# Kernel tuning notes

Measured on AMD Instinct MI355X. Metric: run time of the kernel, lower is better.

The kernel has to match this reference:

```python
import jax, jax.numpy as jnp
import numpy as np

NU, MI, D, H, DH, L, LAYERS = 80000, 40000, 64, 8, 8, 2, 3
EUI, EII, DT, DI, B = 1600000, 400000, 768, 512, 512


def setup_inputs() -> dict:
    rng = np.random.default_rng(0)
    u = rng.integers(0, NU, EUI); it = rng.integers(0, MI, EUI)
    du = np.maximum(np.bincount(u, minlength=NU), 1)
    di = np.maximum(np.bincount(it, minlength=MI), 1)
    val = (1.0 / np.sqrt(du[u] * di[it])).astype(np.float32)
    g_row = np.concatenate([u, it + NU]).astype(np.int32)
    g_col = np.concatenate([it + NU, u]).astype(np.int32)
    g_val = np.concatenate([val, val])

    def ig(seed):  # random item-item graph + self loops (dgl.add_self_loop)
        r = np.random.default_rng(seed)
        s = r.integers(0, MI, EII); d = r.integers(0, MI, EII); sl = np.arange(MI)
        return np.concatenate([s, sl]).astype(np.int32), np.concatenate([d, sl]).astype(np.int32)
    t_src, t_dst = ig(1); i_src, i_dst = ig(2)

    def xav(*shape):
        lim = np.sqrt(6.0 / (shape[-2] + shape[-1]))
        return rng.uniform(-lim, lim, shape).astype(np.float32)

    inp = dict(
        user_emb=(rng.standard_normal((NU, D)) * 0.1).astype(np.float32),
        item_emb=(rng.standard_normal((MI, D)) * 0.1).astype(np.float32),
        g_row=g_row, g_col=g_col, g_val=g_val,
        txt_feat=rng.standard_normal((MI, DT)).astype(np.float32),
        img_feat=rng.standard_normal((MI, DI)).astype(np.float32),
        t_src=t_src, t_dst=t_dst, i_src=i_src, i_dst=i_dst,
        txt_proj_w=xav(DT, D), txt_proj_b=np.zeros(D, np.float32),
        txt_fc_w=xav(L, D, D), txt_attn_l=xav(L, H, DH), txt_attn_r=xav(L, H, DH),
        txt_bias=np.zeros((L, D), np.float32),
        img_proj_w=xav(DI, D), img_proj_b=np.zeros(D, np.float32),
        img_fc_w=xav(L, D, D), img_attn_l=xav(L, H, DH), img_attn_r=xav(L, H, DH),
        img_bias=np.zeros((L, D), np.float32),
        delta_img=xav(D, D), delta_txt=xav(D, D),
        alpha=np.float32(0.05), beta=np.float32(0.8),
        ln_g=np.ones(D, np.float32), ln_b=np.zeros(D, np.float32),
        users=rng.integers(0, NU, B).astype(np.int32),
    )
    return {k: jnp.asarray(v) for k, v in inp.items()}


def _spmm(row, col, val, x, n):
    return jax.ops.segment_sum(val[:, None] * x[col], row, num_segments=n)


def _gat_layer(x, src, dst, fc_w, al, ar, b):
    N = x.shape[0]
    h = (x @ fc_w).reshape(N, H, DH)                 # [N,H,Dh]
    el = jnp.einsum('nhd,hd->nh', h, al)
    er = jnp.einsum('nhd,hd->nh', h, ar)
    e = jax.nn.leaky_relu(el[src] + er[dst], 0.2)    # [E,H]
    m = jax.ops.segment_max(e, dst, num_segments=N)
    a = jnp.exp(e - m[dst])
    a = a / jax.ops.segment_sum(a, dst, num_segments=N)[dst]
    out = jax.ops.segment_sum(a[:, :, None] * h[src], dst, num_segments=N)
    return (out + b.reshape(1, H, DH)).reshape(N, H * DH)


def _branch(feat, src, dst, pw, pb, fcw, al, ar, bias):
    x = feat @ pw + pb
    for l in range(L):
        x = jax.nn.leaky_relu(_gat_layer(x, src, dst, fcw[l], al[l], ar[l], bias[l]), 0.2)
    return x


def _sinkhorn(C, eps=0.01, iters=100):
    K = jnp.exp(-C / eps)
    d1, d2 = C.shape
    mu = jnp.full((d1,), 1.0 / d1, C.dtype)
    nu = jnp.full((d2,), 1.0 / d2, C.dtype)
    def body(_, uv):
        u, v = uv
        u = mu / (K @ v + 1e-8)
        v = nu / (K.T @ u + 1e-8)
        return (u, v)
    u, v = jax.lax.fori_loop(0, iters, body, (mu, nu))
    return u[:, None] * K * v[None, :]


def _ot_align(mm, st, delta):
    I = mm.shape[0]
    # mean_i (mm[i,k]-st[i,l])^2 * scale, without materializing [I,D,D]
    C = ((mm * mm).mean(0)[:, None] + (st * st).mean(0)[None, :] - 2.0 * (mm.T @ st) / I) * 100.0
    T = jax.lax.stop_gradient(_sinkhorn(C))  # torch computes T under no_grad
    return mm @ (T + delta)


def reference(user_emb, item_emb, g_row, g_col, g_val, txt_feat, img_feat,
              t_src, t_dst, i_src, i_dst,
              txt_proj_w, txt_proj_b, txt_fc_w, txt_attn_l, txt_attn_r, txt_bias,
              img_proj_w, img_proj_b, img_fc_w, img_attn_l, img_attn_r, img_bias,
              delta_img, delta_txt, alpha, beta, ln_g, ln_b, users):
    # LightGCN propagation
    cur = jnp.concatenate([user_emb, item_emb], 0)
    acc = cur
    for _ in range(LAYERS):
        cur = _spmm(g_row, g_col, g_val, cur, NU + MI)
        acc = acc + cur
    light = acc / (LAYERS + 1)
    zu, zi_cf = light[:NU], light[NU:]
    # multimodal GAT branches (dropout = eval mode)
    zi_txt = _branch(txt_feat, t_src, t_dst, txt_proj_w, txt_proj_b, txt_fc_w, txt_attn_l, txt_attn_r, txt_bias)
    zi_img = _branch(img_feat, i_src, i_dst, img_proj_w, img_proj_b, img_fc_w, img_attn_l, img_attn_r, img_bias)
    # OAT fusion
    a_img = _ot_align(zi_img, zi_cf, delta_img)
    a_txt = _ot_align(zi_txt, zi_cf, delta_txt)
    z = (1.0 - alpha - beta) * zi_cf + alpha * a_img + beta * a_txt
    mu = z.mean(-1, keepdims=True)
    var = ((z - mu) ** 2).mean(-1, keepdims=True)
    z = (z - mu) / jnp.sqrt(var + 1e-5) * ln_g + ln_b
    z = z / jnp.maximum(jnp.linalg.norm(z, axis=-1, keepdims=True), 1e-12)
    return zu[users] @ z.T  # [B, M_items] ratings
```

## Files before the change

kernel.cpp:

```cpp
#include <hip/hip_runtime.h>
#include <math.h>

__device__ __forceinline__ float lrelu(float x) { return x >= 0.f ? x : 0.2f * x; }

__global__ void hist2_k(const int* __restrict__ d0, const int* __restrict__ d1,
                        int* __restrict__ t0, int* __restrict__ t1, int E) {
  int e = blockIdx.x * 256 + threadIdx.x;
  if (e >= E) return;
  if (blockIdx.y == 0)
    atomicAdd(&t0[d0[e]], 1);
  else
    atomicAdd(&t1[d1[e]], 1);
}

__global__ __launch_bounds__(256) void scan_part2_k(const int* __restrict__ t0,
                                                    const int* __restrict__ t1,
                                                    int* __restrict__ p0,
                                                    int* __restrict__ p1, int N) {
  const int* tick = blockIdx.y ? t1 : t0;
  int* part = blockIdx.y ? p1 : p0;
  __shared__ int red[256];
  int base = blockIdx.x * 4096;
  int s = 0;
  for (int i = threadIdx.x; i < 4096; i += 256) {
    int idx = base + i;
    if (idx < N) s += tick[idx];
  }
  red[threadIdx.x] = s;
  __syncthreads();
  for (int off = 128; off > 0; off >>= 1) {
    if (threadIdx.x < off) red[threadIdx.x] += red[threadIdx.x + off];
    __syncthreads();
  }
  if (threadIdx.x == 0) part[blockIdx.x] = red[0];
}

__global__ __launch_bounds__(1024) void scan_partials2_k(int* __restrict__ p0,
                                                         int* __restrict__ p1, int nb) {
  int* part = blockIdx.y ? p1 : p0;
  __shared__ int sh[1024];
  int t = threadIdx.x;
  int v = (t < nb) ? part[t] : 0;
  sh[t] = v;
  __syncthreads();
  for (int off = 1; off < 1024; off <<= 1) {
    int x = sh[t];
    int y = (t >= off) ? sh[t - off] : 0;
    __syncthreads();
    sh[t] = x + y;
    __syncthreads();
  }
  if (t < nb) part[t] = (t == 0) ? 0 : sh[t - 1];
  if (t == 0) part[nb] = sh[nb - 1];
}

__global__ __launch_bounds__(256) void scan_apply2_k(int* __restrict__ t0, int* __restrict__ t1,
                                                     int* __restrict__ r0, int* __restrict__ r1,
                                                     const int* __restrict__ p0,
                                                     const int* __restrict__ p1, int N, int nb) {
  int* tick = blockIdx.y ? t1 : t0;
  int* rs = blockIdx.y ? r1 : r0;
  const int* part = blockIdx.y ? p1 : p0;
  __shared__ int th[256];
  int base = blockIdx.x * 4096;
  int lo = base + threadIdx.x * 16;
  int vals[16];
  int s = 0;
#pragma unroll
  for (int j = 0; j < 16; ++j) {
    int idx = lo + j;
    int v = (idx < N) ? tick[idx] : 0;
    vals[j] = v;
    s += v;
  }
  th[threadIdx.x] = s;
  __syncthreads();
  for (int off = 1; off < 256; off <<= 1) {
    int x = th[threadIdx.x];
    int y = (threadIdx.x >= off) ? th[threadIdx.x - off] : 0;
    __syncthreads();
    th[threadIdx.x] = x + y;
    __syncthreads();
  }
  int excl = (threadIdx.x == 0) ? 0 : th[threadIdx.x - 1];
  int run = part[blockIdx.x] + excl;
#pragma unroll
  for (int j = 0; j < 16; ++j) {
    int idx = lo + j;
    if (idx < N) {
      rs[idx] = run;
      tick[idx] = run;
      run += vals[j];
    }
  }
  if (blockIdx.x == 0 && threadIdx.x == 0) rs[N] = part[nb];
}

__global__ void scatter_src2_k(const int* __restrict__ s0, const int* __restrict__ d0,
                               const int* __restrict__ s1, const int* __restrict__ d1,
                               int* __restrict__ t0, int* __restrict__ t1,
                               int* __restrict__ o0, int* __restrict__ o1, int E) {
  int e = blockIdx.x * 256 + threadIdx.x;
  if (e >= E) return;
  if (blockIdx.y == 0) {
    int pos = atomicAdd(&t0[d0[e]], 1);
    o0[pos] = s0[e];
  } else {
    int pos = atomicAdd(&t1[d1[e]], 1);
    o1[pos] = s1[e];
  }
}

#define NBUCK_MAX 512

__global__ __launch_bounds__(256) void bin_count_k(const int* __restrict__ row,
                                                   int* __restrict__ bcnt, int E, int nbuck) {
  __shared__ int h[NBUCK_MAX];
  for (int i = threadIdx.x; i < nbuck; i += 256) h[i] = 0;
  __syncthreads();
  int base = blockIdx.x * 4096;
#pragma unroll
  for (int j = 0; j < 16; ++j) {
    int e = base + j * 256 + threadIdx.x;
    if (e < E) atomicAdd(&h[row[e] >> 8], 1);
  }
  __syncthreads();
  for (int i = threadIdx.x; i < nbuck; i += 256) {
    int c = h[i];
    if (c) atomicAdd(&bcnt[i], c);
  }
}

__global__ __launch_bounds__(512) void bucket_scan_k(int* __restrict__ base,
                                                     int* __restrict__ btick, int nbuck) {
  __shared__ int sh[512];
  int t = threadIdx.x;
  int v = (t < nbuck) ? base[t] : 0;
  sh[t] = v;
  __syncthreads();
  for (int off = 1; off < 512; off <<= 1) {
    int x = sh[t];
    int y = (t >= off) ? sh[t - off] : 0;
    __syncthreads();
    sh[t] = x + y;
    __syncthreads();
  }
  if (t < nbuck) {
    int excl = sh[t] - v;
    base[t] = excl;
    btick[t * 16] = excl;
    if (t == nbuck - 1) base[nbuck] = sh[t];
  }
}

__global__ __launch_bounds__(256) void bin_scatter_k(const int* __restrict__ row,
                                                     const int* __restrict__ col,
                                                     const float* __restrict__ val,
                                                     int* __restrict__ btick,
                                                     int* __restrict__ binned, int E, int nbuck) {
  __shared__ int cnt[NBUCK_MAX];
  __shared__ int bbase[NBUCK_MAX];
  for (int i = threadIdx.x; i < nbuck; i += 256) cnt[i] = 0;
  __syncthreads();
  int base = blockIdx.x * 4096;
  int erow[16], rk[16];
#pragma unroll
  for (int j = 0; j < 16; ++j) {
    int e = base + j * 256 + threadIdx.x;
    if (e < E) {
      int r = row[e];
      erow[j] = r;
      rk[j] = atomicAdd(&cnt[r >> 8], 1);
    } else {
      erow[j] = -1;
    }
  }
  __syncthreads();
  for (int i = threadIdx.x; i < nbuck; i += 256) {
    int c = cnt[i];
    bbase[i] = c ? atomicAdd(&btick[i * 16], c) : 0;
  }
  __syncthreads();
#pragma unroll
  for (int j = 0; j < 16; ++j) {
    int e = base + j * 256 + threadIdx.x;
    if (e < E) {
      int r = erow[j];
      int pos = bbase[r >> 8] + rk[j];
      int* p = binned + (size_t)pos * 3;
      p[0] = r;
      p[1] = col[e];
      p[2] = __float_as_int(val[e]);
    }
  }
}

__global__ __launch_bounds__(256) void csr_build_k(const int* __restrict__ bbase,
                                                   const int* __restrict__ binned,
                                                   int* __restrict__ rs,
                                                   int2* __restrict__ cv, int NT) {
  __shared__ int lh[256];
  __shared__ int tmp[256];
  int b = blockIdx.x;
  int t = threadIdx.x;
  int r0 = b << 8;
  int e0 = bbase[b], e1 = bbase[b + 1];
  lh[t] = 0;
  __syncthreads();
  for (int e = e0 + t; e < e1; e += 256) {
    int r = binned[(size_t)e * 3];
    atomicAdd(&lh[r - r0], 1);
  }
  __syncthreads();
  int c = lh[t];
  tmp[t] = c;
  __syncthreads();
  for (int off = 1; off < 256; off <<= 1) {
    int x = tmp[t];
    int y = (t >= off) ? tmp[t - off] : 0;
    __syncthreads();
    tmp[t] = x + y;
    __syncthreads();
  }
  int pos0 = e0 + tmp[t] - c;
  lh[t] = pos0;
  int r = r0 + t;
  if (r < NT) rs[r] = pos0;
  if (t == 0 && b == gridDim.x - 1) rs[NT] = e1;
  __syncthreads();
  for (int e = e0 + t; e < e1; e += 256) {
    const int* p = binned + (size_t)e * 3;
    int rr = p[0];
    int cc = p[1];
    int vv = p[2];
    int pos = atomicAdd(&lh[rr - r0], 1);
    cv[pos] = make_int2(cc, vv);
  }
}

template <int MODE>
__global__ __launch_bounds__(256) void spmm_csr(const int* __restrict__ rs,
                                                const int2* __restrict__ cv,
                                                const float* __restrict__ xs,
                                                const float* __restrict__ ue,
                                                const float* __restrict__ ie, int NUx,
                                                const float* __restrict__ l1,
                                                float* __restrict__ outp, int NT, int wid0) {
  int wid = wid0 + blockIdx.x * 4 + (threadIdx.x >> 6);
  int lane = threadIdx.x & 63;
  if (wid >= NT) return;
  int g = lane >> 4, sl = lane & 15;
  int e0 = rs[wid], e1 = rs[wid + 1];
  double ax = 0.0, ay = 0.0, az = 0.0, aw = 0.0;
  int e = e0;
#define GATHER_PTR(cx)                                                             \
  (MODE == 1 ? ((cx) < NUx ? (const float4*)ue + (size_t)(cx)*16                   \
                           : (const float4*)ie + (size_t)((cx)-NUx) * 16)          \
             : (const float4*)xs + (size_t)(cx)*16)
#define ACC4(vv, xx)                                                               \
  {                                                                                \
    double dv = (double)(vv);                                                      \
    ax += dv * (double)(xx).x;                                                     \
    ay += dv * (double)(xx).y;                                                     \
    az += dv * (double)(xx).z;                                                     \
    aw += dv * (double)(xx).w;                                                     \
  }
  for (; e + 16 <= e1; e += 16) {
    int2 c0 = cv[e + g];
    int2 c1 = cv[e + 4 + g];
    int2 c2 = cv[e + 8 + g];
    int2 c3 = cv[e + 12 + g];
    float4 x0 = GATHER_PTR(c0.x)[sl];
    float4 x1 = GATHER_PTR(c1.x)[sl];
    float4 x2 = GATHER_PTR(c2.x)[sl];
    float4 x3 = GATHER_PTR(c3.x)[sl];
    ACC4(__int_as_float(c0.y), x0);
    ACC4(__int_as_float(c1.y), x1);
    ACC4(__int_as_float(c2.y), x2);
    ACC4(__int_as_float(c3.y), x3);
  }
  for (; e + 4 <= e1; e += 4) {
    int2 c0 = cv[e + g];
    float4 x0 = GATHER_PTR(c0.x)[sl];
    ACC4(__int_as_float(c0.y), x0);
  }
  if (e < e1) {
    int idx = e + g;
    int2 c0 = make_int2(0, 0);
    if (idx < e1) c0 = cv[idx];
    float4 x0 = GATHER_PTR(c0.x)[sl];
    ACC4(__int_as_float(c0.y), x0);
  }
#undef ACC4
#undef GATHER_PTR
  ax += __shfl_xor(ax, 16, 64); ay += __shfl_xor(ay, 16, 64);
  az += __shfl_xor(az, 16, 64); aw += __shfl_xor(aw, 16, 64);
  ax += __shfl_xor(ax, 32, 64); ay += __shfl_xor(ay, 32, 64);
  az += __shfl_xor(az, 32, 64); aw += __shfl_xor(aw, 32, 64);
  if (g == 0) {
    size_t ro = (size_t)wid * 16 + sl;
    float4 s4 = make_float4((float)ax, (float)ay, (float)az, (float)aw);
    if (MODE == 2) {
      float4 x0 = (wid < NUx) ? ((const float4*)ue)[(size_t)wid * 16 + sl]
                              : ((const float4*)ie)[(size_t)(wid - NUx) * 16 + sl];
      float4 f1 = ((const float4*)l1)[ro];
      float4 f2 = ((const float4*)xs)[ro];
      float4 o;
      o.x = (x0.x + f1.x + f2.x + s4.x) * 0.25f;
      o.y = (x0.y + f1.y + f2.y + s4.y) * 0.25f;
      o.z = (x0.z + f1.z + f2.z + s4.z) * 0.25f;
      o.w = (x0.w + f1.w + f2.w + s4.w) * 0.25f;
      ((float4*)outp)[ro] = o;
    } else {
      ((float4*)outp)[ro] = s4;
    }
  }
}

__global__ __launch_bounds__(256) void user_light_k(const int* __restrict__ rs,
                                                    const int2* __restrict__ cv,
                                                    const float* __restrict__ l2,
                                                    const float* __restrict__ ue,
                                                    const float* __restrict__ l1,
                                                    const int* __restrict__ users,
                                                    float* __restrict__ zu, int B) {
  int w = blockIdx.x * 4 + (threadIdx.x >> 6);
  int lane = threadIdx.x & 63;
  if (w >= B) return;
  int u = users[w];
  int g = lane >> 4, sl = lane & 15;
  int e0 = rs[u], e1 = rs[u + 1];
  double ax = 0.0, ay = 0.0, az = 0.0, aw = 0.0;
  int e = e0;
  for (; e + 4 <= e1; e += 4) {
    int2 c0 = cv[e + g];
    float4 x0 = ((const float4*)l2 + (size_t)c0.x * 16)[sl];
    double dv = (double)__int_as_float(c0.y);
    ax += dv * (double)x0.x; ay += dv * (double)x0.y;
    az += dv * (double)x0.z; aw += dv * (double)x0.w;
  }
  if (e < e1) {
    int idx = e + g;
    int2 c0 = make_int2(0, 0);
    if (idx < e1) c0 = cv[idx];
    float4 x0 = ((const float4*)l2 + (size_t)c0.x * 16)[sl];
    double dv = (double)__int_as_float(c0.y);
    ax += dv * (double)x0.x; ay += dv * (double)x0.y;
    az += dv * (double)x0.z; aw += dv * (double)x0.w;
  }
  ax += __shfl_xor(ax, 16, 64); ay += __shfl_xor(ay, 16, 64);
  az += __shfl_xor(az, 16, 64); aw += __shfl_xor(aw, 16, 64);
  ax += __shfl_xor(ax, 32, 64); ay += __shfl_xor(ay, 32, 64);
  az += __shfl_xor(az, 32, 64); aw += __shfl_xor(aw, 32, 64);
  if (g == 0) {
    size_t ro = (size_t)u * 16 + sl;
    float4 x0 = ((const float4*)ue)[ro];
    float4 f1 = ((const float4*)l1)[ro];
    float4 f2 = ((const float4*)l2)[ro];
    float4 o;
    o.x = (x0.x + f1.x + f2.x + (float)ax) * 0.25f;
    o.y = (x0.y + f1.y + f2.y + (float)ay) * 0.25f;
    o.z = (x0.z + f1.z + f2.z + (float)az) * 0.25f;
    o.w = (x0.w + f1.w + f2.w + (float)aw) * 0.25f;
    ((float4*)zu)[(size_t)w * 16 + sl] = o;
  }
}

template <int ACT>
__global__ __launch_bounds__(256) void gemm2_n64(const float* __restrict__ A0,
                                                 const float* __restrict__ A1,
                                                 const float* __restrict__ W0,
                                                 const float* __restrict__ W1,
                                                 const float* __restrict__ b0,
                                                 const float* __restrict__ b1,
                                                 float* __restrict__ C0,
                                                 float* __restrict__ C1, int M, int K0, int K1) {
  const float* A = blockIdx.y ? A1 : A0;
  const float* W = blockIdx.y ? W1 : W0;
  const float* bias = blockIdx.y ? b1 : b0;
  float* C = blockIdx.y ? C1 : C0;
  const int K = blockIdx.y ? K1 : K0;
  __shared__ float AsT[32][132];
  __shared__ float Ws[32][64];
  int t = threadIdx.x;
  int row0 = blockIdx.x * 128;
  int tr = t >> 4, tc = t & 15;
  int lr = t >> 1, lq = (t & 1) * 16;
  int wk = t >> 3, wc = (t & 7) * 8;
  float acc[8][4] = {};
  for (int k0 = 0; k0 < K; k0 += 32) {
    float a16[16];
    if (row0 + lr < M) {
      const float* src = A + (size_t)(row0 + lr) * K + k0 + lq;
#pragma unroll
      for (int j = 0; j < 16; j += 4) {
        float4 v = *(const float4*)(src + j);
        a16[j] = v.x; a16[j + 1] = v.y; a16[j + 2] = v.z; a16[j + 3] = v.w;
      }
    } else {
#pragma unroll
      for (int i = 0; i < 16; ++i) a16[i] = 0.f;
    }
    float4 w0 = *(const float4*)(W + (size_t)(k0 + wk) * 64 + wc);
    float4 w1 = *(const float4*)(W + (size_t)(k0 + wk) * 64 + wc + 4);
    __syncthreads();
#pragma unroll
    for (int i = 0; i < 16; ++i) AsT[lq + i][lr] = a16[i];
    *(float4*)&Ws[wk][wc] = w0;
    *(float4*)&Ws[wk][wc + 4] = w1;
    __syncthreads();
#pragma unroll
    for (int kki = 0; kki < 32; ++kki) {
      float4 av0 = *(const float4*)&AsT[kki][tr * 8];
      float4 av1 = *(const float4*)&AsT[kki][tr * 8 + 4];
      float4 wv = *(const float4*)&Ws[kki][tc * 4];
      acc[0][0] += av0.x * wv.x; acc[0][1] += av0.x * wv.y;
      acc[0][2] += av0.x * wv.z; acc[0][3] += av0.x * wv.w;
      acc[1][0] += av0.y * wv.x; acc[1][1] += av0.y * wv.y;
      acc[1][2] += av0.y * wv.z; acc[1][3] += av0.y * wv.w;
      acc[2][0] += av0.z * wv.x; acc[2][1] += av0.z * wv.y;
      acc[2][2] += av0.z * wv.z; acc[2][3] += av0.z * wv.w;
      acc[3][0] += av0.w * wv.x; acc[3][1] += av0.w * wv.y;
      acc[3][2] += av0.w * wv.z; acc[3][3] += av0.w * wv.w;
      acc[4][0] += av1.x * wv.x; acc[4][1] += av1.x * wv.y;
      acc[4][2] += av1.x * wv.z; acc[4][3] += av1.x * wv.w;
      acc[5][0] += av1.y * wv.x; acc[5][1] += av1.y * wv.y;
      acc[5][2] += av1.y * wv.z; acc[5][3] += av1.y * wv.w;
      acc[6][0] += av1.z * wv.x; acc[6][1] += av1.z * wv.y;
      acc[6][2] += av1.z * wv.z; acc[6][3] += av1.z * wv.w;
      acc[7][0] += av1.w * wv.x; acc[7][1] += av1.w * wv.y;
      acc[7][2] += av1.w * wv.z; acc[7][3] += av1.w * wv.w;
    }
  }
  float bv[4] = {0.f, 0.f, 0.f, 0.f};
  if (bias) *(float4*)bv = *(const float4*)(bias + tc * 4);
#pragma unroll
  for (int j = 0; j < 8; ++j) {
    int row = row0 + tr * 8 + j;
    if (row < M) {
      float o[4];
#pragma unroll
      for (int c = 0; c < 4; ++c) {
        float x = acc[j][c] + bv[c];
        o[c] = ACT ? lrelu(x) : x;
      }
      *(float4*)(C + (size_t)row * 64 + tc * 4) = *(float4*)o;
    }
  }
}

__global__ void attn2_scores(const float* __restrict__ h0, const float* __restrict__ h1,
                             const float* __restrict__ al0, const float* __restrict__ al1,
                             const float* __restrict__ ar0, const float* __restrict__ ar1,
                             float* __restrict__ el0, float* __restrict__ el1,
                             float* __restrict__ er0, float* __restrict__ er1, int N) {
  long t = (long)blockIdx.x * blockDim.x + threadIdx.x;
  if (t >= (long)N * 8) return;
  const float* h = blockIdx.y ? h1 : h0;
  const float* al = blockIdx.y ? al1 : al0;
  const float* ar = blockIdx.y ? ar1 : ar0;
  float* el = blockIdx.y ? el1 : el0;
  float* er = blockIdx.y ? er1 : er0;
  int n = (int)(t >> 3), hh = (int)(t & 7);
  const float4* hp = (const float4*)(h + (size_t)n * 64 + hh * 8);
  float4 hv0 = hp[0], hv1 = hp[1];
  const float4* ap = (const float4*)(al + hh * 8);
  float4 a0 = ap[0], a1 = ap[1];
  const float4* bp = (const float4*)(ar + hh * 8);
  float4 b0 = bp[0], b1 = bp[1];
  float sl = hv0.x * a0.x + hv0.y * a0.y + hv0.z * a0.z + hv0.w * a0.w +
             hv1.x * a1.x + hv1.y * a1.y + hv1.z * a1.z + hv1.w * a1.w;
  float sr = hv0.x * b0.x + hv0.y * b0.y + hv0.z * b0.z + hv0.w * b0.w +
             hv1.x * b1.x + hv1.y * b1.y + hv1.z * b1.z + hv1.w * b1.w;
  el[t] = sl;
  er[t] = sr;
}

__global__ __launch_bounds__(256) void gat_agg2(const int* __restrict__ rsa,
                                                const int* __restrict__ rsb,
                                                const int* __restrict__ sa,
                                                const int* __restrict__ sb,
                                                const float* __restrict__ ela,
                                                const float* __restrict__ elb,
                                                const float* __restrict__ era,
                                                const float* __restrict__ erb,
                                                const float* __restrict__ ha,
                                                const float* __restrict__ hbp,
                                                const float* __restrict__ ba,
                                                const float* __restrict__ bb,
                                                float* __restrict__ oa,
                                                float* __restrict__ ob, int N) {
  int br = blockIdx.y;
  const int* rs = br ? rsb : rsa;
  const int* srcs = br ? sb : sa;
  const float* el = br ? elb : ela;
  const float* er = br ? erb : era;
  const float* h = br ? hbp : ha;
  const float* bias = br ? bb : ba;
  float* out = br ? ob : oa;
  int d = blockIdx.x * 4 + (threadIdx.x >> 6);
  int lane = threadIdx.x & 63;
  if (d >= N) return;
  int hh = lane >> 3;
  int e0 = rs[d], e1 = rs[d + 1];
  float erd = er[(size_t)d * 8 + hh];
  double den = 0.0, acc = 0.0;
  int e = e0;
  for (; e + 8 <= e1; e += 8) {
    int s8[8];
#pragma unroll
    for (int j = 0; j < 8; ++j) s8[j] = srcs[e + j];
    float v8[8];
#pragma unroll
    for (int j = 0; j < 8; ++j) v8[j] = el[(size_t)s8[j] * 8 + hh];
    float h8[8];
#pragma unroll
    for (int j = 0; j < 8; ++j) h8[j] = h[(size_t)s8[j] * 64 + lane];
#pragma unroll
    for (int j = 0; j < 8; ++j) {
      float a = expf(lrelu(v8[j] + erd));
      den += (double)a;
      acc += (double)a * (double)h8[j];
    }
  }
  for (; e < e1; ++e) {
    int s = srcs[e];
    float a = expf(lrelu(el[(size_t)s * 8 + hh] + erd));
    den += (double)a;
    acc += (double)a * (double)h[(size_t)s * 64 + lane];
  }
  out[(size_t)d * 64 + lane] = lrelu((float)(acc / den) + bias[lane]);
}

__global__ __launch_bounds__(256) void gram_part_k(const float* __restrict__ mm0,
                                                   const float* __restrict__ mm1,
                                                   const float* __restrict__ st,
                                                   float* __restrict__ part, int N) {
  __shared__ float ms[128][64];
  __shared__ float ss[128][64];
  const float* mm = blockIdx.y ? mm1 : mm0;
  float* po = part + ((size_t)blockIdx.y * gridDim.x + blockIdx.x) * 4224;
  int t = threadIdx.x;
  int n0 = blockIdx.x * 128;
  for (int idx = t; idx < 128 * 16; idx += 256) {
    int r = idx >> 4, q = (idx & 15) * 4;
    float4 a, b;
    if (n0 + r < N) {
      a = *(const float4*)(mm + (size_t)(n0 + r) * 64 + q);
      b = *(const float4*)(st + (size_t)(n0 + r) * 64 + q);
    } else {
      a = make_float4(0, 0, 0, 0);
      b = make_float4(0, 0, 0, 0);
    }
    *(float4*)&ms[r][q] = a;
    *(float4*)&ss[r][q] = b;
  }
  __syncthreads();
  if (t < 64) {
    float s = 0.f;
    for (int n = 0; n < 128; ++n) { float x = ms[n][t]; s += x * x; }
    po[4096 + t] = s;
  } else if (t < 128) {
    int c = t - 64;
    float s = 0.f;
    for (int n = 0; n < 128; ++n) { float x = ss[n][c]; s += x * x; }
    po[4160 + c] = s;
  }
  int i = t >> 2, jb = (t & 3) * 16;
  float acc[16] = {};
  for (int n = 0; n < 128; ++n) {
    float a = ms[n][i];
#pragma unroll
    for (int j = 0; j < 16; ++j) acc[j] += a * ss[n][jb + j];
  }
#pragma unroll
  for (int j = 0; j < 16; j += 4)
    *(float4*)&po[i * 64 + jb + j] = *(float4*)&acc[j];
}

__global__ __launch_bounds__(256) void gram_reduce_k(const float* __restrict__ part,
                                                     double* __restrict__ G_all, int nb) {
  int idx = blockIdx.x * 256 + threadIdx.x;
  if (idx >= 4224) return;
  int br = blockIdx.y;
  const float* p = part + (size_t)br * nb * 4224 + idx;
  double s = 0.0;
  int b = 0;
  for (; b + 4 <= nb; b += 4) {
    s += ((double)p[(size_t)b * 4224] + (double)p[(size_t)(b + 1) * 4224]) +
         ((double)p[(size_t)(b + 2) * 4224] + (double)p[(size_t)(b + 3) * 4224]);
  }
  for (; b < nb; ++b) s += (double)p[(size_t)b * 4224];
  G_all[(size_t)br * 4224 + idx] = s;
}

__global__ __launch_bounds__(256) void sinkhorn2_k(const double* __restrict__ G_all,
                                                   const float* __restrict__ delta_txt,
                                                   const float* __restrict__ delta_img,
                                                   float* __restrict__ TD_all, int N) {
  __shared__ double u_s[64], v_s[64];
  int b = blockIdx.x;
  const double* G = G_all + (size_t)b * 4224;
  const double* mmsq = G + 4096;
  const double* stsq = G + 4160;
  const float* delta = b ? delta_img : delta_txt;
  float* TD = TD_all + (size_t)b * 4096;
  int t = threadIdx.x;
  int r = t >> 2, p = t & 3;
  int j0 = p * 16;
  double invN = 1.0 / (double)N;
  double Kr[16], Kc[16];
  double rq = mmsq[r] * invN;
  double cq = stsq[r] * invN;
#pragma unroll
  for (int q = 0; q < 16; ++q) {
    int j = j0 + q;
    double Crj = (rq + stsq[j] * invN - 2.0 * G[r * 64 + j] * invN) * 100.0;
    Kr[q] = exp(-Crj / 0.01);
    double Cjr = (mmsq[j] * invN + cq - 2.0 * G[j * 64 + r] * invN) * 100.0;
    Kc[q] = exp(-Cjr / 0.01);
  }
  if (p == 0) {
    u_s[r] = 1.0 / 64.0;
    v_s[r] = 1.0 / 64.0;
  }
  __syncthreads();
  for (int it = 0; it < 100; ++it) {
    double s0 = 0.0, s1 = 0.0, s2 = 0.0, s3 = 0.0;
#pragma unroll
    for (int q = 0; q < 16; q += 4) {
      s0 += Kr[q] * v_s[j0 + q];
      s1 += Kr[q + 1] * v_s[j0 + q + 1];
      s2 += Kr[q + 2] * v_s[j0 + q + 2];
      s3 += Kr[q + 3] * v_s[j0 + q + 3];
    }
    double s = (s0 + s1) + (s2 + s3);
    s += __shfl_xor(s, 1, 64);
    s += __shfl_xor(s, 2, 64);
    if (p == 0) u_s[r] = (1.0 / 64.0) / (s + 1e-8);
    __syncthreads();
    double z0 = 0.0, z1 = 0.0, z2 = 0.0, z3 = 0.0;
#pragma unroll
    for (int q = 0; q < 16; q += 4) {
      z0 += Kc[q] * u_s[j0 + q];
      z1 += Kc[q + 1] * u_s[j0 + q + 1];
      z2 += Kc[q + 2] * u_s[j0 + q + 2];
      z3 += Kc[q + 3] * u_s[j0 + q + 3];
    }
    double z = (z0 + z1) + (z2 + z3);
    z += __shfl_xor(z, 1, 64);
    z += __shfl_xor(z, 2, 64);
    if (p == 0) v_s[r] = (1.0 / 64.0) / (z + 1e-8);
    __syncthreads();
  }
  double ur = u_s[r];
#pragma unroll
  for (int q = 0; q < 16; ++q) {
    int j = j0 + q;
    TD[r * 64 + j] = (float)(ur * Kr[q] * v_s[j]) + delta[r * 64 + j];
  }
}

__global__ __launch_bounds__(256) void fuse_ln(const float* __restrict__ zi_cf,
                                               const float* __restrict__ a_img,
                                               const float* __restrict__ a_txt,
                                               const float* __restrict__ g,
                                               const float* __restrict__ b,
                                               const float* __restrict__ alpha_p,
                                               const float* __restrict__ beta_p,
                                               float* __restrict__ z, int N) {
  long gt = (long)blockIdx.x * blockDim.x + threadIdx.x;
  long row = gt >> 6;
  int lane = (int)(gt & 63);
  if (row >= N) return;
  float al = *alpha_p, be = *beta_p;
  size_t idx = (size_t)row * 64 + lane;
  float v = (1.f - al - be) * zi_cf[idx] + al * a_img[idx] + be * a_txt[idx];
  float s = v;
  for (int o = 32; o; o >>= 1) s += __shfl_xor(s, o, 64);
  float mean = s * (1.f / 64.f);
  float dv = v - mean;
  float q = dv * dv;
  for (int o = 32; o; o >>= 1) q += __shfl_xor(q, o, 64);
  float var = q * (1.f / 64.f);
  float zn = dv / sqrtf(var + 1e-5f) * g[lane] + b[lane];
  float n2 = zn * zn;
  for (int o = 32; o; o >>= 1) n2 += __shfl_xor(n2, o, 64);
  float nrm = fmaxf(sqrtf(n2), 1e-12f);
  z[idx] = zn / nrm;
}

__global__ __launch_bounds__(256) void final_gemm(const float* __restrict__ zu,
                                                  const float* __restrict__ z,
                                                  float* __restrict__ out, int B, int NI) {
  __shared__ float zu_s[64][65];
  __shared__ float zs_s[64][65];
  int t = threadIdx.x;
  int i0 = blockIdx.x * 64;
  int b0 = blockIdx.y * 64;
  {
    int r = t >> 2, q = (t & 3) * 16;
    float vals[16];
    if (b0 + r < B) {
      const float* src = zu + (size_t)(b0 + r) * 64 + q;
#pragma unroll
      for (int j = 0; j < 16; j += 4) {
        float4 v = *(const float4*)(src + j);
        vals[j] = v.x; vals[j + 1] = v.y; vals[j + 2] = v.z; vals[j + 3] = v.w;
      }
    } else {
#pragma unroll
      for (int j = 0; j < 16; ++j) vals[j] = 0.f;
    }
#pragma unroll
    for (int j = 0; j < 16; ++j) zu_s[r][q + j] = vals[j];
    const float* zsrc = z + (size_t)(i0 + r) * 64 + q;
#pragma unroll
    for (int j = 0; j < 16; j += 4) {
      float4 v = *(const float4*)(zsrc + j);
      zs_s[r][q + j] = v.x; zs_s[r][q + j + 1] = v.y;
      zs_s[r][q + j + 2] = v.z; zs_s[r][q + j + 3] = v.w;
    }
  }
  __syncthreads();
  int tu = t >> 4, tc = t & 15;
  float acc[4][4] = {};
  for (int d = 0; d < 64; ++d) {
    float au[4], zv[4];
#pragma unroll
    for (int j = 0; j < 4; ++j) au[j] = zu_s[tu * 4 + j][d];
#pragma unroll
    for (int j = 0; j < 4; ++j) zv[j] = zs_s[tc * 4 + j][d];
#pragma unroll
    for (int j = 0; j < 4; ++j)
#pragma unroll
      for (int k = 0; k < 4; ++k) acc[j][k] += au[j] * zv[k];
  }
#pragma unroll
  for (int j = 0; j < 4; ++j) {
    int bb = b0 + tu * 4 + j;
    if (bb < B) {
      float4 o = make_float4(acc[j][0], acc[j][1], acc[j][2], acc[j][3]);
      *(float4*)(out + (size_t)bb * NI + i0 + tc * 4) = o;
    }
  }
}

static inline int cdiv_i(long a, long b) { return (int)((a + b - 1) / b); }

extern "C" void kernel_launch(void* const* d_in, const int* in_sizes, int n_in,
                              void* d_out, int out_size, void* d_ws, size_t ws_size,
                              hipStream_t stream) {
  const float* user_emb = (const float*)d_in[0];
  const float* item_emb = (const float*)d_in[1];
  const int* g_row = (const int*)d_in[2];
  const int* g_col = (const int*)d_in[3];
  const float* g_val = (const float*)d_in[4];
  const float* txt_feat = (const float*)d_in[5];
  const float* img_feat = (const float*)d_in[6];
  const int* t_src = (const int*)d_in[7];
  const int* t_dst = (const int*)d_in[8];
  const int* i_src = (const int*)d_in[9];
  const int* i_dst = (const int*)d_in[10];
  const float* txt_proj_w = (const float*)d_in[11];
  const float* txt_proj_b = (const float*)d_in[12];
  const float* txt_fc_w = (const float*)d_in[13];
  const float* txt_attn_l = (const float*)d_in[14];
  const float* txt_attn_r = (const float*)d_in[15];
  const float* txt_bias = (const float*)d_in[16];
  const float* img_proj_w = (const float*)d_in[17];
  const float* img_proj_b = (const float*)d_in[18];
  const float* img_fc_w = (const float*)d_in[19];
  const float* img_attn_l = (const float*)d_in[20];
  const float* img_attn_r = (const float*)d_in[21];
  const float* img_bias = (const float*)d_in[22];
  const float* delta_img = (const float*)d_in[23];
  const float* delta_txt = (const float*)d_in[24];
  const float* alpha = (const float*)d_in[25];
  const float* beta = (const float*)d_in[26];
  const float* ln_g = (const float*)d_in[27];
  const float* ln_b = (const float*)d_in[28];
  const int* users = (const int*)d_in[29];

  const int NU = in_sizes[0] / 64;
  const int MI = in_sizes[1] / 64;
  const int EG = in_sizes[2];
  const int DT = in_sizes[5] / MI;
  const int DI = in_sizes[6] / MI;
  const int ET = in_sizes[7];
  const int B = in_sizes[29];
  const int NT = NU + MI;
  const size_t NT64 = (size_t)NT * 64;
  const size_t MI64 = (size_t)MI * 64;
  const size_t MI8 = (size_t)MI * 8;

  float* cur = (float*)d_ws;
  float* nxt = cur + NT64;
  int* rs = (int*)(nxt + NT64);
  int* tick = rs + (NT + 1);
  int2* cv = (int2*)(tick + (NT + 1));
  int* rs_g = (int*)(cv + EG);
  int* tick_g = rs_g + (MI + 1);
  int* gat_src = tick_g + (MI + 1);
  int* part = gat_src + ET;
  float* TD_all = (float*)(part + 1025);
  uintptr_t gaddr = ((uintptr_t)(TD_all + 8192) + 15) & ~(uintptr_t)15;
  double* G_all = (double*)gaddr;
  float* zu_sel = (float*)(G_all + 2 * 4224);

  float* acc = (float*)d_out;
  float* base2 = (float*)d_out + NT64;
  float* xb2 = base2;
  float* hb2 = base2 + MI64;
  float* el2 = base2 + 2 * MI64;
  float* er2 = el2 + MI8;
  int* ints2 = (int*)(er2 + MI8);
  int* rs_g2 = ints2;
  int* tick_g2 = rs_g2 + (MI + 1);
  int* gat_src2 = tick_g2 + (MI + 1);
  int* part2 = gat_src2 + ET;

  float* xb = cur;
  float* hb = cur + MI64;
  float* el = cur + 2 * MI64;
  float* er = el + MI8;
  float* zi_txt = nxt + MI64;
  float* zi_img = nxt + 2 * MI64;
  float* a_txt = cur;
  float* a_img = cur + MI64;
  float* zbuf = nxt;

  const int nbuck = (NT + 255) >> 8;
  int* binned = (int*)cur;
  int* btick = binned + (((size_t)3 * EG + 15) & ~(size_t)15);
  int* bbase = part;
  hipMemsetAsync(bbase, 0, (nbuck + 1) * sizeof(int), stream);
  bin_count_k<<<cdiv_i(EG, 4096), 256, 0, stream>>>(g_row, bbase, EG, nbuck);
  bucket_scan_k<<<1, 512, 0, stream>>>(bbase, btick, nbuck);
  bin_scatter_k<<<cdiv_i(EG, 4096), 256, 0, stream>>>(g_row, g_col, g_val, btick, binned, EG,
                                                      nbuck);
  csr_build_k<<<nbuck, 256, 0, stream>>>(bbase, binned, rs, cv, NT);

  const int spmmGrid = cdiv_i(NT, 4);
  spmm_csr<1><<<spmmGrid, 256, 0, stream>>>(rs, cv, nullptr, user_emb, item_emb, NU,
                                            nullptr, cur, NT, 0);
  spmm_csr<0><<<spmmGrid, 256, 0, stream>>>(rs, cv, cur, nullptr, nullptr, 0,
                                            nullptr, nxt, NT, 0);
  spmm_csr<2><<<cdiv_i(MI, 4), 256, 0, stream>>>(rs, cv, nxt, user_emb, item_emb, NU,
                                                 cur, acc, NT, NU);
  user_light_k<<<cdiv_i(B, 4), 256, 0, stream>>>(rs, cv, nxt, user_emb, cur, users, zu_sel, B);
  const float* zi_cf = acc + (size_t)NU * 64;

  const int gemmGrid = cdiv_i(MI, 128);
  const int aggGrid = cdiv_i(MI, 4);
  const int nbg = cdiv_i(MI, 4096);

  hipMemsetAsync(tick_g, 0, (MI + 1) * sizeof(int), stream);
  hipMemsetAsync(tick_g2, 0, (MI + 1) * sizeof(int), stream);
  {
    dim3 eh(cdiv_i(ET, 256), 2);
    dim3 sp(nbg, 2);
    hist2_k<<<eh, 256, 0, stream>>>(t_dst, i_dst, tick_g, tick_g2, ET);
    scan_part2_k<<<sp, 256, 0, stream>>>(tick_g, tick_g2, part, part2, MI);
    scan_partials2_k<<<dim3(1, 2), 1024, 0, stream>>>(part, part2, nbg);
    scan_apply2_k<<<sp, 256, 0, stream>>>(tick_g, tick_g2, rs_g, rs_g2, part, part2, MI, nbg);
    scatter_src2_k<<<eh, 256, 0, stream>>>(t_src, t_dst, i_src, i_dst, tick_g, tick_g2,
                                           gat_src, gat_src2, ET);
  }
  {
    dim3 gg(gemmGrid, 2);
    dim3 ag(aggGrid, 2);
    dim3 at(cdiv_i((long)MI * 8, 256), 2);
    gemm2_n64<0><<<gg, 256, 0, stream>>>(txt_feat, img_feat, txt_proj_w, img_proj_w,
                                         txt_proj_b, img_proj_b, xb, xb2, MI, DT, DI);
    for (int l = 0; l < 2; ++l) {
      gemm2_n64<0><<<gg, 256, 0, stream>>>(xb, xb2, txt_fc_w + l * 4096, img_fc_w + l * 4096,
                                           nullptr, nullptr, hb, hb2, MI, 64, 64);
      attn2_scores<<<at, 256, 0, stream>>>(hb, hb2, txt_attn_l + l * 64, img_attn_l + l * 64,
                                           txt_attn_r + l * 64, img_attn_r + l * 64,
                                           el, el2, er, er2, MI);
      gat_agg2<<<ag, 256, 0, stream>>>(rs_g, rs_g2, gat_src, gat_src2, el, el2, er, er2,
                                       hb, hb2, txt_bias + l * 64, img_bias + l * 64,
                                       (l == 1) ? zi_txt : xb, (l == 1) ? zi_img : xb2, MI);
    }
  }

  const int ngb = cdiv_i(MI, 128);
  float* gpart = cur;
  {
    dim3 gg(ngb, 2);
    gram_part_k<<<gg, 256, 0, stream>>>(zi_txt, zi_img, zi_cf, gpart, MI);
    dim3 rg(cdiv_i(4224, 256), 2);
    gram_reduce_k<<<rg, 256, 0, stream>>>(gpart, G_all, ngb);
  }
  sinkhorn2_k<<<2, 256, 0, stream>>>(G_all, delta_txt, delta_img, TD_all, MI);
  {
    dim3 gg(gemmGrid, 2);
    gemm2_n64<0><<<gg, 256, 0, stream>>>(zi_txt, zi_img, TD_all, TD_all + 4096, nullptr, nullptr,
                                         a_txt, a_img, MI, 64, 64);
  }

  fuse_ln<<<cdiv_i((long)MI * 64, 256), 256, 0, stream>>>(zi_cf, a_img, a_txt, ln_g, ln_b, alpha,
                                                          beta, zbuf, MI);

  dim3 fg(MI / 64, cdiv_i(B, 64));
  final_gemm<<<fg, 256, 0, stream>>>(zu_sel, zbuf, (float*)d_out, B, MI);
}
```

Baseline: 994.5 us.

## Split-K input projection GEMMs and shrink fc GEMM tile to 64 rows

The input projection GEMMs (K=768 and K=512) are split into 256-wide K chunks, each writing partial outputs, and a separate reduce kernel sums the chunks and adds the bias. This gives the GPU more blocks to run in parallel than the 313x2 grid did. The per-layer fc GEMM (K=64) now uses 64-row tiles with a 4x4 per-thread micro-tile, doubling its block count. The cost is extra partial-buffer traffic, one more kernel launch, and new scratch buffers carved from existing workspace, which could overlap live data.

```diff
diff --git a/kernel.cpp b/kernel.cpp
--- a/kernel.cpp
+++ b/kernel.cpp
@@ -380,15 +380,88 @@
   const float* bias = blockIdx.y ? b1 : b0;
   float* C = blockIdx.y ? C1 : C0;
   const int K = blockIdx.y ? K1 : K0;
+  __shared__ float AsT[32][68];
+  __shared__ float Ws[32][64];
+  int t = threadIdx.x;
+  int row0 = blockIdx.x * 64;
+  int tr = t >> 4, tc = t & 15;
+  int lr = t >> 2, lq = (t & 3) * 8;
+  float acc[4][4] = {};
+  for (int k0 = 0; k0 < K; k0 += 32) {
+    float a8[8];
+    if (row0 + lr < M) {
+      const float* src = A + (size_t)(row0 + lr) * K + k0 + lq;
+      float4 v0 = *(const float4*)(src);
+      float4 v1 = *(const float4*)(src + 4);
+      a8[0] = v0.x; a8[1] = v0.y; a8[2] = v0.z; a8[3] = v0.w;
+      a8[4] = v1.x; a8[5] = v1.y; a8[6] = v1.z; a8[7] = v1.w;
+    } else {
+#pragma unroll
+      for (int i = 0; i < 8; ++i) a8[i] = 0.f;
+    }
+    const float4* wsrc = (const float4*)(W + (size_t)k0 * 64);
+    float4 w0 = wsrc[t];
+    float4 w1 = wsrc[t + 256];
+    __syncthreads();
+#pragma unroll
+    for (int i = 0; i < 8; ++i) AsT[lq + i][lr] = a8[i];
+    ((float4*)Ws)[t] = w0;
+    ((float4*)Ws)[t + 256] = w1;
+    __syncthreads();
+#pragma unroll
+    for (int kki = 0; kki < 32; ++kki) {
+      float4 av = *(const float4*)&AsT[kki][tr * 4];
+      float4 wv = *(const float4*)&Ws[kki][tc * 4];
+      acc[0][0] += av.x * wv.x; acc[0][1] += av.x * wv.y;
+      acc[0][2] += av.x * wv.z; acc[0][3] += av.x * wv.w;
+      acc[1][0] += av.y * wv.x; acc[1][1] += av.y * wv.y;
+      acc[1][2] += av.y * wv.z; acc[1][3] += av.y * wv.w;
+      acc[2][0] += av.z * wv.x; acc[2][1] += av.z * wv.y;
+      acc[2][2] += av.z * wv.z; acc[2][3] += av.z * wv.w;
+      acc[3][0] += av.w * wv.x; acc[3][1] += av.w * wv.y;
+      acc[3][2] += av.w * wv.z; acc[3][3] += av.w * wv.w;
+    }
+  }
+  float bv[4] = {0.f, 0.f, 0.f, 0.f};
+  if (bias) *(float4*)bv = *(const float4*)(bias + tc * 4);
+#pragma unroll
+  for (int j = 0; j < 4; ++j) {
+    int row = row0 + tr * 4 + j;
+    if (row < M) {
+      float o[4];
+#pragma unroll
+      for (int c = 0; c < 4; ++c) {
+        float x = acc[j][c] + bv[c];
+        o[c] = ACT ? lrelu(x) : x;
+      }
+      *(float4*)(C + (size_t)row * 64 + tc * 4) = *(float4*)o;
+    }
+  }
+}
+
+__global__ __launch_bounds__(256) void gemm_ksplit_k(const float* __restrict__ A0,
+                                                     const float* __restrict__ A1,
+                                                     const float* __restrict__ W0,
+                                                     const float* __restrict__ W1,
+                                                     float* __restrict__ P0,
+                                                     float* __restrict__ P1,
+                                                     int M, int K0, int K1, int nc0) {
+  int y = blockIdx.y;
+  int br = (y >= nc0) ? 1 : 0;
+  int chunk = br ? (y - nc0) : y;
+  const float* A = br ? A1 : A0;
+  const float* W = br ? W1 : W0;
+  const int K = br ? K1 : K0;
+  float* P = (br ? P1 : P0) + (size_t)chunk * M * 64;
+  const int kbeg = chunk * 256;
   __shared__ float AsT[32][132];
   __shared__ float Ws[32][64];
   int t = threadIdx.x;
   int row0 = blockIdx.x * 128;
   int tr = t >> 4, tc = t & 15;
   int lr = t >> 1, lq = (t & 1) * 16;
-  int wk = t >> 3, wc = (t & 7) * 8;
   float acc[8][4] = {};
-  for (int k0 = 0; k0 < K; k0 += 32) {
+  for (int k0 = kbeg; k0 < kbeg + 256; k0 += 32) {
     float a16[16];
     if (row0 + lr < M) {
       const float* src = A + (size_t)(row0 + lr) * K + k0 + lq;
@@ -401,13 +474,14 @@
 #pragma unroll
       for (int i = 0; i < 16; ++i) a16[i] = 0.f;
     }
-    float4 w0 = *(const float4*)(W + (size_t)(k0 + wk) * 64 + wc);
-    float4 w1 = *(const float4*)(W + (size_t)(k0 + wk) * 64 + wc + 4);
+    const float4* wsrc = (const float4*)(W + (size_t)k0 * 64);
+    float4 w0 = wsrc[t];
+    float4 w1 = wsrc[t + 256];
     __syncthreads();
 #pragma unroll
     for (int i = 0; i < 16; ++i) AsT[lq + i][lr] = a16[i];
-    *(float4*)&Ws[wk][wc] = w0;
-    *(float4*)&Ws[wk][wc + 4] = w1;
+    ((float4*)Ws)[t] = w0;
+    ((float4*)Ws)[t + 256] = w1;
     __syncthreads();
 #pragma unroll
     for (int kki = 0; kki < 32; ++kki) {
@@ -432,20 +506,45 @@
       acc[7][2] += av1.w * wv.z; acc[7][3] += av1.w * wv.w;
     }
   }
-  float bv[4] = {0.f, 0.f, 0.f, 0.f};
-  if (bias) *(float4*)bv = *(const float4*)(bias + tc * 4);
 #pragma unroll
   for (int j = 0; j < 8; ++j) {
     int row = row0 + tr * 8 + j;
-    if (row < M) {
-      float o[4];
-#pragma unroll
-      for (int c = 0; c < 4; ++c) {
-        float x = acc[j][c] + bv[c];
-        o[c] = ACT ? lrelu(x) : x;
-      }
-      *(float4*)(C + (size_t)row * 64 + tc * 4) = *(float4*)o;
-    }
+    if (row < M)
+      *(float4*)(P + (size_t)row * 64 + tc * 4) = *(float4*)acc[j];
+  }
+}
+
+__global__ __launch_bounds__(256) void proj_reduce_k(const float* __restrict__ P0,
+                                                     const float* __restrict__ P1,
+                                                     const float* __restrict__ b0,
+                                                     const float* __restrict__ b1,
+                                                     float* __restrict__ C0,
+                                                     float* __restrict__ C1, long M) {
+  long i = (long)blockIdx.x * 256 + threadIdx.x;
+  long n4 = M * 16;
+  if (i >= n4) return;
+  int col4 = (int)(i & 15);
+  if (blockIdx.y == 0) {
+    float4 a = ((const float4*)P0)[i];
+    float4 b = ((const float4*)P0)[i + n4];
+    float4 c = ((const float4*)P0)[i + 2 * n4];
+    float4 bb = ((const float4*)b0)[col4];
+    float4 o;
+    o.x = ((a.x + b.x) + c.x) + bb.x;
+    o.y = ((a.y + b.y) + c.y) + bb.y;
+    o.z = ((a.z + b.z) + c.z) + bb.z;
+    o.w = ((a.w + b.w) + c.w) + bb.w;
+    ((float4*)C0)[i] = o;
+  } else {
+    float4 a = ((const float4*)P1)[i];
+    float4 b = ((const float4*)P1)[i + n4];
+    float4 bb = ((const float4*)b1)[col4];
+    float4 o;
+    o.x = (a.x + b.x) + bb.x;
+    o.y = (a.y + b.y) + bb.y;
+    o.z = (a.z + b.z) + bb.z;
+    o.w = (a.w + b.w) + bb.w;
+    ((float4*)C1)[i] = o;
   }
 }
 
@@ -819,6 +918,8 @@
   int* tick_g2 = rs_g2 + (MI + 1);
   int* gat_src2 = tick_g2 + (MI + 1);
   int* part2 = gat_src2 + ET;
+  uintptr_t pimaddr = ((uintptr_t)(part2 + 1025) + 15) & ~(uintptr_t)15;
+  float* pimg = (float*)pimaddr;
 
   float* xb = cur;
   float* hb = cur + MI64;
@@ -829,6 +930,7 @@
   float* a_txt = cur;
   float* a_img = cur + MI64;
   float* zbuf = nxt;
+  float* ptxt = nxt;
 
   const int nbuck = (NT + 255) >> 8;
   int* binned = (int*)cur;
@@ -851,7 +953,7 @@
   user_light_k<<<cdiv_i(B, 4), 256, 0, stream>>>(rs, cv, nxt, user_emb, cur, users, zu_sel, B);
   const float* zi_cf = acc + (size_t)NU * 64;
 
-  const int gemmGrid = cdiv_i(MI, 128);
+  const int gemmGrid = cdiv_i(MI, 64);
   const int aggGrid = cdiv_i(MI, 4);
   const int nbg = cdiv_i(MI, 4096);
 
@@ -868,11 +970,16 @@
                                            gat_src, gat_src2, ET);
   }
   {
+    const int nc0 = DT / 256, nc1 = DI / 256;
+    dim3 kg(cdiv_i(MI, 128), nc0 + nc1);
+    gemm_ksplit_k<<<kg, 256, 0, stream>>>(txt_feat, img_feat, txt_proj_w, img_proj_w,
+                                          ptxt, pimg, MI, DT, DI, nc0);
+    dim3 rg(cdiv_i((long)MI * 16, 256), 2);
+    proj_reduce_k<<<rg, 256, 0, stream>>>(ptxt, pimg, txt_proj_b, img_proj_b, xb, xb2, MI);
+
     dim3 gg(gemmGrid, 2);
     dim3 ag(aggGrid, 2);
     dim3 at(cdiv_i((long)MI * 8, 256), 2);
-    gemm2_n64<0><<<gg, 256, 0, stream>>>(txt_feat, img_feat, txt_proj_w, img_proj_w,
-                                         txt_proj_b, img_proj_b, xb, xb2, MI, DT, DI);
     for (int l = 0; l < 2; ++l) {
       gemm2_n64<0><<<gg, 256, 0, stream>>>(xb, xb2, txt_fc_w + l * 4096, img_fc_w + l * 4096,
                                            nullptr, nullptr, hb, hb2, MI, 64, 64);
```

Measured after the change: 1.017 ms. +2.2%, slower.
